# Kernel optimization log

Measured on AMD Instinct MI355X. Metric: run time of the kernel, lower is better.

## Reference

```python
import jax, jax.numpy as jnp
import numpy as np

N = 50000      # nodes
E = 800000     # edges (before self-loops)
H = 4          # attention heads
C = 32         # out_features per head
DIN = 128      # in_features (== H*C so residual path is active)
ED = 16        # edge_dim
NEG = 0.2      # LeakyReLU negative slope (GATConv default)
EPS = 1e-5     # LayerNorm eps


def setup_inputs() -> dict:
    key = jax.random.key(0)
    ks = jax.random.split(key, 12)
    s = 0.05
    return {
        "x": jax.random.normal(ks[0], (N, DIN), dtype=jnp.float32),
        "edge_index": jax.random.randint(ks[1], (2, E), 0, N, dtype=jnp.int64),
        "edge_attr": jax.random.normal(ks[2], (E, ED), dtype=jnp.float32),
        # edge_processor: Linear(ED, ED) + ReLU (dropout = identity at eval)
        "W_ep": jax.random.normal(ks[3], (ED, ED), dtype=jnp.float32) * s,
        "b_ep": jnp.zeros((ED,), dtype=jnp.float32),
        # GATConv params (lin / lin_edge are bias-free in PyG)
        "W_lin": jax.random.normal(ks[4], (DIN, H * C), dtype=jnp.float32) * s,
        "W_edge": jax.random.normal(ks[5], (ED, H * C), dtype=jnp.float32) * s,
        "att_src": jax.random.normal(ks[6], (H, C), dtype=jnp.float32) * s,
        "att_dst": jax.random.normal(ks[7], (H, C), dtype=jnp.float32) * s,
        "att_edge": jax.random.normal(ks[8], (H, C), dtype=jnp.float32) * s,
        "bias": jnp.zeros((H * C,), dtype=jnp.float32),
        # LayerNorm params
        "ln_g": jnp.ones((H * C,), dtype=jnp.float32),
        "ln_b": jnp.zeros((H * C,), dtype=jnp.float32),
    }


def reference(x, edge_index, edge_attr, W_ep, b_ep, W_lin, W_edge,
              att_src, att_dst, att_edge, bias, ln_g, ln_b):
    n = x.shape[0]
    src, dst = edge_index[0], edge_index[1]

    # edge_processor: Linear + ReLU
    ea = jax.nn.relu(edge_attr @ W_ep + b_ep)                       # [E, ED]

    # add self-loops (PyG GATConv default), loop edge_attr = mean of incoming
    ones = jnp.ones((ea.shape[0],), dtype=ea.dtype)
    deg = jax.ops.segment_sum(ones, dst, num_segments=n)            # [N]
    loop_attr = jax.ops.segment_sum(ea, dst, num_segments=n)
    loop_attr = loop_attr / jnp.maximum(deg, 1.0)[:, None]          # [N, ED]
    loop = jnp.arange(n, dtype=src.dtype)
    src2 = jnp.concatenate([src, loop])                             # [E+N]
    dst2 = jnp.concatenate([dst, loop])
    ea2 = jnp.concatenate([ea, loop_attr], axis=0)                  # [E+N, ED]

    # node / edge linear transforms
    h = (x @ W_lin).reshape(n, H, C)                                # [N, H, C]
    a_src = jnp.einsum('nhc,hc->nh', h, att_src)                    # [N, H]
    a_dst = jnp.einsum('nhc,hc->nh', h, att_dst)
    e = (ea2 @ W_edge).reshape(-1, H, C)                            # [E+N, H, C]
    a_e = jnp.einsum('ehc,hc->eh', e, att_edge)                     # [E+N, H]

    # per-edge attention logits + leaky relu
    alpha = a_src[src2] + a_dst[dst2] + a_e                         # [E+N, H]
    alpha = jnp.where(alpha >= 0, alpha, NEG * alpha)

    # segment softmax over incoming edges of each dst node
    m = jax.ops.segment_max(alpha, dst2, num_segments=n)            # [N, H]
    ex = jnp.exp(alpha - m[dst2])
    denom = jax.ops.segment_sum(ex, dst2, num_segments=n)           # [N, H]
    w = ex / denom[dst2]                                            # [E+N, H]

    # scatter-aggregate messages
    msg = h[src2] * w[:, :, None]                                   # [E+N, H, C]
    out = jax.ops.segment_sum(msg, dst2, num_segments=n)            # [N, H, C]
    out = out.reshape(n, H * C) + bias

    # residual (DIN == H*C) + LayerNorm
    out = out + x
    mu = jnp.mean(out, axis=-1, keepdims=True)
    var = jnp.var(out, axis=-1, keepdims=True)
    out = (out - mu) * jax.lax.rsqrt(var + EPS) * ln_g + ln_b
    return out
```

## Files before the change

### kernel.cpp

```cpp
#include <hip/hip_runtime.h>
#include <hip/hip_fp16.h>
#include <math.h>

#define NN   50000
#define EE   800000
#define HH   4
#define CC   32
#define DINN 128
#define ED   16
#define NEGS 0.2f
#define LNEPS 1e-5f
#define CPAD 32
#define SLOT 64
#define SLOTP (SLOT + 4)

struct __align__(16) Hp4 { __half2 a, b, c, d; };

__global__ __launch_bounds__(256, 4) void k_node(
        const float* __restrict__ x, const float* __restrict__ W_lin,
        const float* __restrict__ att_src, const float* __restrict__ att_dst,
        __half* __restrict__ hb, float* __restrict__ a_src, float* __restrict__ a_dst,
        int* __restrict__ cnt) {
    __shared__ float xr[64 * 132];
    int t = threadIdx.x;
    int row0 = blockIdx.x * 64;

    #pragma unroll
    for (int i = 0; i < 8; ++i) {
        int idx = blockIdx.x * 2048 + i * 256 + t;
        if (idx < NN * CPAD) cnt[idx] = 0;
    }

    #pragma unroll
    for (int i = 0; i < 8; ++i) {
        int idx = t + 256 * i;
        int r = idx >> 5, kq = idx & 31;
        int row = row0 + r;
        float4 v = make_float4(0.f, 0.f, 0.f, 0.f);
        if (row < NN) v = ((const float4*)x)[(long)row * 32 + kq];
        *(float4*)&xr[r * 132 + kq * 4] = v;
    }
    __syncthreads();

    int colg = t & 15, rowg = t >> 4;
    int c0 = colg * 8;
    const float* Wp = W_lin + c0;
    float acc[4][8] = {};

    #pragma unroll 2
    for (int k = 0; k < DINN; k += 2) {
        float4 wa0 = *(const float4*)&Wp[(long)k * DINN];
        float4 wb0 = *(const float4*)&Wp[(long)k * DINN + 4];
        float4 wa1 = *(const float4*)&Wp[(long)(k + 1) * DINN];
        float4 wb1 = *(const float4*)&Wp[(long)(k + 1) * DINN + 4];
        #pragma unroll
        for (int i = 0; i < 4; ++i) {
            float2 xv = *(const float2*)&xr[(rowg * 4 + i) * 132 + k];
            acc[i][0] = fmaf(xv.x, wa0.x, acc[i][0]);
            acc[i][1] = fmaf(xv.x, wa0.y, acc[i][1]);
            acc[i][2] = fmaf(xv.x, wa0.z, acc[i][2]);
            acc[i][3] = fmaf(xv.x, wa0.w, acc[i][3]);
            acc[i][4] = fmaf(xv.x, wb0.x, acc[i][4]);
            acc[i][5] = fmaf(xv.x, wb0.y, acc[i][5]);
            acc[i][6] = fmaf(xv.x, wb0.z, acc[i][6]);
            acc[i][7] = fmaf(xv.x, wb0.w, acc[i][7]);
            acc[i][0] = fmaf(xv.y, wa1.x, acc[i][0]);
            acc[i][1] = fmaf(xv.y, wa1.y, acc[i][1]);
            acc[i][2] = fmaf(xv.y, wa1.z, acc[i][2]);
            acc[i][3] = fmaf(xv.y, wa1.w, acc[i][3]);
            acc[i][4] = fmaf(xv.y, wb1.x, acc[i][4]);
            acc[i][5] = fmaf(xv.y, wb1.y, acc[i][5]);
            acc[i][6] = fmaf(xv.y, wb1.z, acc[i][6]);
            acc[i][7] = fmaf(xv.y, wb1.w, acc[i][7]);
        }
    }

    int head = colg >> 2;
    int cw = c0 & 31;
    float4 as0 = *(const float4*)&att_src[head * CC + cw];
    float4 as1 = *(const float4*)&att_src[head * CC + cw + 4];
    float4 ad0 = *(const float4*)&att_dst[head * CC + cw];
    float4 ad1 = *(const float4*)&att_dst[head * CC + cw + 4];
    #pragma unroll
    for (int i = 0; i < 4; ++i) {
        int row = row0 + rowg * 4 + i;
        if (row < NN) {
            Hp4 p;
            p.a = __floats2half2_rn(acc[i][0], acc[i][1]);
            p.b = __floats2half2_rn(acc[i][2], acc[i][3]);
            p.c = __floats2half2_rn(acc[i][4], acc[i][5]);
            p.d = __floats2half2_rn(acc[i][6], acc[i][7]);
            *(Hp4*)&hb[(long)row * DINN + c0] = p;
        }
        float ps = acc[i][0]*as0.x + acc[i][1]*as0.y + acc[i][2]*as0.z + acc[i][3]*as0.w
                 + acc[i][4]*as1.x + acc[i][5]*as1.y + acc[i][6]*as1.z + acc[i][7]*as1.w;
        float pd = acc[i][0]*ad0.x + acc[i][1]*ad0.y + acc[i][2]*ad0.z + acc[i][3]*ad0.w
                 + acc[i][4]*ad1.x + acc[i][5]*ad1.y + acc[i][6]*ad1.z + acc[i][7]*ad1.w;
        ps += __shfl_xor(ps, 1); ps += __shfl_xor(ps, 2);
        pd += __shfl_xor(pd, 1); pd += __shfl_xor(pd, 2);
        if ((colg & 3) == 0 && row < NN) {
            a_src[row * 4 + head] = ps;
            a_dst[row * 4 + head] = pd;
        }
    }
}

__device__ __forceinline__ void edge_compute(
        float4 A0, float4 A1, float4 A2, float4 A3,
        const float* __restrict__ Wl, const float* __restrict__ bl,
        const float* __restrict__ vl,
        int e, uint2* __restrict__ payload) {
    float a[ED];
    a[0]=A0.x; a[1]=A0.y; a[2]=A0.z; a[3]=A0.w;
    a[4]=A1.x; a[5]=A1.y; a[6]=A1.z; a[7]=A1.w;
    a[8]=A2.x; a[9]=A2.y; a[10]=A2.z; a[11]=A2.w;
    a[12]=A3.x; a[13]=A3.y; a[14]=A3.z; a[15]=A3.w;

    float r[ED];
    #pragma unroll
    for (int j = 0; j < ED; ++j) r[j] = bl[j];
    #pragma unroll
    for (int d = 0; d < ED; ++d) {
        float av = a[d];
        #pragma unroll
        for (int j = 0; j < ED; ++j) r[j] = fmaf(av, Wl[d * ED + j], r[j]);
    }

    float ae0 = 0.f, ae1 = 0.f, ae2 = 0.f, ae3 = 0.f;
    #pragma unroll
    for (int d = 0; d < ED; ++d) {
        float rd = fmaxf(r[d], 0.f);
        ae0 = fmaf(rd, vl[d * 4 + 0], ae0);
        ae1 = fmaf(rd, vl[d * 4 + 1], ae1);
        ae2 = fmaf(rd, vl[d * 4 + 2], ae2);
        ae3 = fmaf(rd, vl[d * 4 + 3], ae3);
    }

    __half2 ae01 = __floats2half2_rn(ae0, ae1);
    __half2 ae23 = __floats2half2_rn(ae2, ae3);
    payload[e] = make_uint2(*(unsigned*)&ae01, *(unsigned*)&ae23);
}

__global__ __launch_bounds__(256) void k_edgeA(
        const int* __restrict__ ei, const float* __restrict__ edge_attr,
        const float* __restrict__ W_ep, const float* __restrict__ b_ep,
        const float* __restrict__ W_edge, const float* __restrict__ att_edge,
        int* __restrict__ cnt, uint2* __restrict__ payload,
        uint2* __restrict__ bkt) {
    __shared__ float Wl[ED * ED];
    __shared__ float bl[ED];
    __shared__ float vl[ED * 4];
    int t = threadIdx.x;
    if (t < ED * ED) Wl[t] = W_ep[t];
    if (t < ED) bl[t] = b_ep[t];
    if (t >= 192 && t < 192 + 64) {
        int q = t - 192;
        int d = q >> 2, h = q & 3;
        float s = 0.f;
        #pragma unroll 8
        for (int c = 0; c < CC; ++c)
            s += W_edge[d * (HH * CC) + h * CC + c] * att_edge[h * CC + c];
        vl[q] = s;
    }
    __syncthreads();

    int e0 = blockIdx.x * 512 + t;
    int e1 = e0 + 256;

    if ((blockIdx.x + 1) * 512 <= EE) {
        int s0 = ei[e0], s1 = ei[e1];
        int d0 = ei[EE + e0], d1 = ei[EE + e1];

        const float4* ap0 = (const float4*)(edge_attr + (long)e0 * ED);
        const float4* ap1 = (const float4*)(edge_attr + (long)e1 * ED);
        float4 A0 = ap0[0], A1 = ap0[1], A2 = ap0[2], A3 = ap0[3];
        float4 B0 = ap1[0], B1 = ap1[1], B2 = ap1[2], B3 = ap1[3];

        int rk0 = atomicAdd(cnt + (long)d0 * CPAD, 1);
        int rk1 = atomicAdd(cnt + (long)d1 * CPAD, 1);

        if (rk0 < SLOT) bkt[(long)d0 * SLOT + rk0] = make_uint2((unsigned)e0, (unsigned)s0);
        if (rk1 < SLOT) bkt[(long)d1 * SLOT + rk1] = make_uint2((unsigned)e1, (unsigned)s1);

        edge_compute(A0, A1, A2, A3, Wl, bl, vl, e0, payload);
        edge_compute(B0, B1, B2, B3, Wl, bl, vl, e1, payload);
    } else {
        #pragma unroll
        for (int u = 0; u < 2; ++u) {
            int e = e0 + u * 256;
            if (e >= EE) break;
            int src = ei[e];
            int dst = ei[EE + e];
            const float4* ap = (const float4*)(edge_attr + (long)e * ED);
            float4 A0 = ap[0], A1 = ap[1], A2 = ap[2], A3 = ap[3];
            int rk = atomicAdd(cnt + (long)dst * CPAD, 1);
            if (rk < SLOT) bkt[(long)dst * SLOT + rk] = make_uint2((unsigned)e, (unsigned)src);
            edge_compute(A0, A1, A2, A3, Wl, bl, vl, e, payload);
        }
    }
}

__global__ __launch_bounds__(256) void k_aggregate(
        const float* __restrict__ x, const __half2* __restrict__ hb,
        const float* __restrict__ a_src, const float* __restrict__ a_dst,
        const int* __restrict__ cnt, const uint2* __restrict__ payload,
        const uint2* __restrict__ bkt,
        const float* __restrict__ bias, const float* __restrict__ ln_g,
        const float* __restrict__ ln_b, float* __restrict__ out) {
    __shared__ float2 wa[4][HH][SLOTP];
    __shared__ int    sl[4][SLOT];
    int t = threadIdx.x;
    int wave = t >> 6, lane = t & 63;
    int n = blockIdx.x * 4 + wave;

    int deg = cnt[(long)n * CPAD];
    if (deg > SLOT) deg = SLOT;
    int head = lane >> 4;

    float4 ad4 = *(const float4*)&a_dst[n * 4];

    if (lane < deg) {
        uint2 b = bkt[(long)n * SLOT + lane];
        int eidx = (int)b.x;
        int src  = (int)b.y;
        uint2 q = payload[eidx];
        float4 as4 = *(const float4*)&a_src[src * 4];
        float2 a01 = __half22float2(*(__half2*)&q.x);
        float2 a23 = __half22float2(*(__half2*)&q.y);
        float v0 = as4.x + ad4.x + a01.x; v0 = (v0 >= 0.f) ? v0 : NEGS * v0;
        float v1 = as4.y + ad4.y + a01.y; v1 = (v1 >= 0.f) ? v1 : NEGS * v1;
        float v2 = as4.z + ad4.z + a23.x; v2 = (v2 >= 0.f) ? v2 : NEGS * v2;
        float v3 = as4.w + ad4.w + a23.y; v3 = (v3 >= 0.f) ? v3 : NEGS * v3;
        wa[wave][0][lane] = make_float2(__expf(v0), a01.x);
        wa[wave][1][lane] = make_float2(__expf(v1), a01.y);
        wa[wave][2][lane] = make_float2(__expf(v2), a23.x);
        wa[wave][3][lane] = make_float2(__expf(v3), a23.y);
        sl[wave][lane] = src;
    }
    __syncthreads();

    const float2* wp = &wa[wave][head][0];
    const int*    sp = &sl[wave][0];
    float accx = 0.f, accy = 0.f, s_own = 0.f, aes_own = 0.f;

    int k = 0;
    for (; k + 8 <= deg; k += 8) {
        int s0 = sp[k+0], s1 = sp[k+1], s2 = sp[k+2], s3 = sp[k+3];
        int s4 = sp[k+4], s5 = sp[k+5], s6 = sp[k+6], s7 = sp[k+7];
        float2 W0 = wp[k+0], W1 = wp[k+1], W2 = wp[k+2], W3 = wp[k+3];
        float2 W4 = wp[k+4], W5 = wp[k+5], W6 = wp[k+6], W7 = wp[k+7];
        __half2 h0 = hb[(long)s0 * 64 + lane], h1 = hb[(long)s1 * 64 + lane];
        __half2 h2 = hb[(long)s2 * 64 + lane], h3 = hb[(long)s3 * 64 + lane];
        __half2 h4 = hb[(long)s4 * 64 + lane], h5 = hb[(long)s5 * 64 + lane];
        __half2 h6 = hb[(long)s6 * 64 + lane], h7 = hb[(long)s7 * 64 + lane];
        float2 f0 = __half22float2(h0), f1 = __half22float2(h1);
        float2 f2 = __half22float2(h2), f3 = __half22float2(h3);
        float2 f4 = __half22float2(h4), f5 = __half22float2(h5);
        float2 f6 = __half22float2(h6), f7 = __half22float2(h7);
        s_own += W0.x; aes_own += W0.y;
        accx = fmaf(W0.x, f0.x, accx); accy = fmaf(W0.x, f0.y, accy);
        s_own += W1.x; aes_own += W1.y;
        accx = fmaf(W1.x, f1.x, accx); accy = fmaf(W1.x, f1.y, accy);
        s_own += W2.x; aes_own += W2.y;
        accx = fmaf(W2.x, f2.x, accx); accy = fmaf(W2.x, f2.y, accy);
        s_own += W3.x; aes_own += W3.y;
        accx = fmaf(W3.x, f3.x, accx); accy = fmaf(W3.x, f3.y, accy);
        s_own += W4.x; aes_own += W4.y;
        accx = fmaf(W4.x, f4.x, accx); accy = fmaf(W4.x, f4.y, accy);
        s_own += W5.x; aes_own += W5.y;
        accx = fmaf(W5.x, f5.x, accx); accy = fmaf(W5.x, f5.y, accy);
        s_own += W6.x; aes_own += W6.y;
        accx = fmaf(W6.x, f6.x, accx); accy = fmaf(W6.x, f6.y, accy);
        s_own += W7.x; aes_own += W7.y;
        accx = fmaf(W7.x, f7.x, accx); accy = fmaf(W7.x, f7.y, accy);
    }
    for (; k < deg; ++k) {
        int s0 = sp[k];
        float2 W0 = wp[k];
        __half2 h0 = hb[(long)s0 * 64 + lane];
        float2 f0 = __half22float2(h0);
        s_own += W0.x; aes_own += W0.y;
        accx = fmaf(W0.x, f0.x, accx); accy = fmaf(W0.x, f0.y, accy);
    }

    float adn = (head & 2) ? ((head & 1) ? ad4.w : ad4.z)
                           : ((head & 1) ? ad4.y : ad4.x);
    float asn = a_src[n * 4 + head];
    float inv_deg = 1.0f / fmaxf((float)deg, 1.0f);
    float v = asn + adn + aes_own * inv_deg;
    v = (v >= 0.f) ? v : NEGS * v;
    float w0 = __expf(v);
    s_own += w0;
    float2 hn = __half22float2(hb[(long)n * 64 + lane]);
    accx = fmaf(w0, hn.x, accx);
    accy = fmaf(w0, hn.y, accy);
    float is = 1.0f / s_own;
    accx *= is; accy *= is;

    int c0 = lane * 2;
    float2 b2 = *(const float2*)&bias[c0];
    float2 x2 = *(const float2*)&x[(long)n * DINN + c0];
    float oa = accx + b2.x + x2.x;
    float ob = accy + b2.y + x2.y;
    float sum = oa + ob, sumsq = oa * oa + ob * ob;
    #pragma unroll
    for (int d2 = 1; d2 < 64; d2 <<= 1) {
        sum   += __shfl_xor(sum, d2);
        sumsq += __shfl_xor(sumsq, d2);
    }
    float mu  = sum * (1.0f / DINN);
    float var = sumsq * (1.0f / DINN) - mu * mu;
    float rs  = rsqrtf(var + LNEPS);
    float2 g2  = *(const float2*)&ln_g[c0];
    float2 lb2 = *(const float2*)&ln_b[c0];
    float2 o2;
    o2.x = (oa - mu) * rs * g2.x + lb2.x;
    o2.y = (ob - mu) * rs * g2.y + lb2.y;
    *(float2*)&out[(long)n * DINN + c0] = o2;
}

extern "C" void kernel_launch(void* const* d_in, const int* in_sizes, int n_in,
                              void* d_out, int out_size, void* d_ws, size_t ws_size,
                              hipStream_t stream) {
    const float* x         = (const float*)d_in[0];
    const int*   ei        = (const int*)d_in[1];
    const float* edge_attr = (const float*)d_in[2];
    const float* W_ep      = (const float*)d_in[3];
    const float* b_ep      = (const float*)d_in[4];
    const float* W_lin     = (const float*)d_in[5];
    const float* W_edge    = (const float*)d_in[6];
    const float* att_src   = (const float*)d_in[7];
    const float* att_dst   = (const float*)d_in[8];
    const float* att_edge  = (const float*)d_in[9];
    const float* bias      = (const float*)d_in[10];
    const float* ln_g      = (const float*)d_in[11];
    const float* ln_b      = (const float*)d_in[12];
    float* out = (float*)d_out;

    char* ws = (char*)d_ws;
    size_t o = 0;
    auto take = [&](size_t bytes) -> char* {
        char* p = ws + o;
        o = (o + bytes + 255) & ~(size_t)255;
        return p;
    };
    __half* hbuf    = (__half*)take((size_t)NN * DINN * 2);
    float*  a_src   = (float*)take((size_t)NN * 4 * 4);
    float*  a_dst   = (float*)take((size_t)NN * 4 * 4);
    int*    cnt     = (int*)  take((size_t)NN * CPAD * 4);
    uint2*  payload = (uint2*)take((size_t)EE * 8);
    uint2*  bkt     = (uint2*)take((size_t)NN * SLOT * 8);

    k_node<<<(NN + 63) / 64, 256, 0, stream>>>(x, W_lin, att_src, att_dst,
                                               hbuf, a_src, a_dst, cnt);
    k_edgeA<<<(EE + 511) / 512, 256, 0, stream>>>(ei, edge_attr, W_ep, b_ep,
                                                  W_edge, att_edge, cnt,
                                                  payload, bkt);
    k_aggregate<<<(NN + 3) / 4, 256, 0, stream>>>(x, (const __half2*)hbuf,
                                                  a_src, a_dst, cnt,
                                                  payload, bkt,
                                                  bias, ln_g, ln_b, out);
}
```

Baseline: 255.6 us.

## Fuse edge MLP attention logit computation into aggregation kernel

The per-edge Linear+ReLU and attention-edge projection moves out of the bucketing kernel and into the aggregation kernel. Each gathered incoming edge now reads its raw edge_attr row and computes its logit in place, so the fp16 payload array no longer has to be written and then read back. The bucketing kernel shrinks to index loads and atomics only. In exchange, aggregation does a random 64-byte gather per edge instead of an 8-byte one, and its register pressure rises from the 16x16 MLP.

```diff
diff --git a/kernel.cpp b/kernel.cpp
--- a/kernel.cpp
+++ b/kernel.cpp
@@ -105,52 +105,51 @@
     }
 }
 
-__device__ __forceinline__ void edge_compute(
-        float4 A0, float4 A1, float4 A2, float4 A3,
-        const float* __restrict__ Wl, const float* __restrict__ bl,
-        const float* __restrict__ vl,
-        int e, uint2* __restrict__ payload) {
-    float a[ED];
-    a[0]=A0.x; a[1]=A0.y; a[2]=A0.z; a[3]=A0.w;
-    a[4]=A1.x; a[5]=A1.y; a[6]=A1.z; a[7]=A1.w;
-    a[8]=A2.x; a[9]=A2.y; a[10]=A2.z; a[11]=A2.w;
-    a[12]=A3.x; a[13]=A3.y; a[14]=A3.z; a[15]=A3.w;
-
-    float r[ED];
-    #pragma unroll
-    for (int j = 0; j < ED; ++j) r[j] = bl[j];
-    #pragma unroll
-    for (int d = 0; d < ED; ++d) {
-        float av = a[d];
-        #pragma unroll
-        for (int j = 0; j < ED; ++j) r[j] = fmaf(av, Wl[d * ED + j], r[j]);
-    }
-
-    float ae0 = 0.f, ae1 = 0.f, ae2 = 0.f, ae3 = 0.f;
-    #pragma unroll
-    for (int d = 0; d < ED; ++d) {
-        float rd = fmaxf(r[d], 0.f);
-        ae0 = fmaf(rd, vl[d * 4 + 0], ae0);
-        ae1 = fmaf(rd, vl[d * 4 + 1], ae1);
-        ae2 = fmaf(rd, vl[d * 4 + 2], ae2);
-        ae3 = fmaf(rd, vl[d * 4 + 3], ae3);
-    }
-
-    __half2 ae01 = __floats2half2_rn(ae0, ae1);
-    __half2 ae23 = __floats2half2_rn(ae2, ae3);
-    payload[e] = make_uint2(*(unsigned*)&ae01, *(unsigned*)&ae23);
+__global__ __launch_bounds__(256) void k_bkt(
+        const int* __restrict__ ei, int* __restrict__ cnt,
+        uint2* __restrict__ bkt) {
+    int t = threadIdx.x;
+    int e0 = blockIdx.x * 512 + t;
+    int e1 = e0 + 256;
+
+    if ((blockIdx.x + 1) * 512 <= EE) {
+        int s0 = ei[e0], s1 = ei[e1];
+        int d0 = ei[EE + e0], d1 = ei[EE + e1];
+        int rk0 = atomicAdd(cnt + (long)d0 * CPAD, 1);
+        int rk1 = atomicAdd(cnt + (long)d1 * CPAD, 1);
+        if (rk0 < SLOT) bkt[(long)d0 * SLOT + rk0] = make_uint2((unsigned)e0, (unsigned)s0);
+        if (rk1 < SLOT) bkt[(long)d1 * SLOT + rk1] = make_uint2((unsigned)e1, (unsigned)s1);
+    } else {
+        #pragma unroll
+        for (int u = 0; u < 2; ++u) {
+            int e = e0 + u * 256;
+            if (e >= EE) break;
+            int src = ei[e];
+            int dst = ei[EE + e];
+            int rk = atomicAdd(cnt + (long)dst * CPAD, 1);
+            if (rk < SLOT) bkt[(long)dst * SLOT + rk] = make_uint2((unsigned)e, (unsigned)src);
+        }
+    }
 }
 
-__global__ __launch_bounds__(256) void k_edgeA(
-        const int* __restrict__ ei, const float* __restrict__ edge_attr,
+__global__ __launch_bounds__(256) void k_aggregate(
+        const float* __restrict__ x, const __half2* __restrict__ hb,
+        const float* __restrict__ a_src, const float* __restrict__ a_dst,
+        const int* __restrict__ cnt, const float* __restrict__ edge_attr,
+        const uint2* __restrict__ bkt,
         const float* __restrict__ W_ep, const float* __restrict__ b_ep,
         const float* __restrict__ W_edge, const float* __restrict__ att_edge,
-        int* __restrict__ cnt, uint2* __restrict__ payload,
-        uint2* __restrict__ bkt) {
-    __shared__ float Wl[ED * ED];
-    __shared__ float bl[ED];
-    __shared__ float vl[ED * 4];
+        const float* __restrict__ bias, const float* __restrict__ ln_g,
+        const float* __restrict__ ln_b, float* __restrict__ out) {
+    __shared__ float2 wa[4][HH][SLOTP];
+    __shared__ int    sl[4][SLOT];
+    __shared__ float  Wl[ED * ED];
+    __shared__ float  bl[ED];
+    __shared__ float  vl[ED * 4];
     int t = threadIdx.x;
+    int wave = t >> 6, lane = t & 63;
+    int n = blockIdx.x * 4 + wave;
+
     if (t < ED * ED) Wl[t] = W_ep[t];
     if (t < ED) bl[t] = b_ep[t];
     if (t >= 192 && t < 192 + 64) {
@@ -162,79 +161,56 @@
             s += W_edge[d * (HH * CC) + h * CC + c] * att_edge[h * CC + c];
         vl[q] = s;
     }
-    __syncthreads();
-
-    int e0 = blockIdx.x * 512 + t;
-    int e1 = e0 + 256;
-
-    if ((blockIdx.x + 1) * 512 <= EE) {
-        int s0 = ei[e0], s1 = ei[e1];
-        int d0 = ei[EE + e0], d1 = ei[EE + e1];
-
-        const float4* ap0 = (const float4*)(edge_attr + (long)e0 * ED);
-        const float4* ap1 = (const float4*)(edge_attr + (long)e1 * ED);
-        float4 A0 = ap0[0], A1 = ap0[1], A2 = ap0[2], A3 = ap0[3];
-        float4 B0 = ap1[0], B1 = ap1[1], B2 = ap1[2], B3 = ap1[3];
-
-        int rk0 = atomicAdd(cnt + (long)d0 * CPAD, 1);
-        int rk1 = atomicAdd(cnt + (long)d1 * CPAD, 1);
-
-        if (rk0 < SLOT) bkt[(long)d0 * SLOT + rk0] = make_uint2((unsigned)e0, (unsigned)s0);
-        if (rk1 < SLOT) bkt[(long)d1 * SLOT + rk1] = make_uint2((unsigned)e1, (unsigned)s1);
-
-        edge_compute(A0, A1, A2, A3, Wl, bl, vl, e0, payload);
-        edge_compute(B0, B1, B2, B3, Wl, bl, vl, e1, payload);
-    } else {
-        #pragma unroll
-        for (int u = 0; u < 2; ++u) {
-            int e = e0 + u * 256;
-            if (e >= EE) break;
-            int src = ei[e];
-            int dst = ei[EE + e];
-            const float4* ap = (const float4*)(edge_attr + (long)e * ED);
-            float4 A0 = ap[0], A1 = ap[1], A2 = ap[2], A3 = ap[3];
-            int rk = atomicAdd(cnt + (long)dst * CPAD, 1);
-            if (rk < SLOT) bkt[(long)dst * SLOT + rk] = make_uint2((unsigned)e, (unsigned)src);
-            edge_compute(A0, A1, A2, A3, Wl, bl, vl, e, payload);
-        }
-    }
-}
-
-__global__ __launch_bounds__(256) void k_aggregate(
-        const float* __restrict__ x, const __half2* __restrict__ hb,
-        const float* __restrict__ a_src, const float* __restrict__ a_dst,
-        const int* __restrict__ cnt, const uint2* __restrict__ payload,
-        const uint2* __restrict__ bkt,
-        const float* __restrict__ bias, const float* __restrict__ ln_g,
-        const float* __restrict__ ln_b, float* __restrict__ out) {
-    __shared__ float2 wa[4][HH][SLOTP];
-    __shared__ int    sl[4][SLOT];
-    int t = threadIdx.x;
-    int wave = t >> 6, lane = t & 63;
-    int n = blockIdx.x * 4 + wave;
 
     int deg = cnt[(long)n * CPAD];
     if (deg > SLOT) deg = SLOT;
     int head = lane >> 4;
 
     float4 ad4 = *(const float4*)&a_dst[n * 4];
+    __syncthreads();
 
     if (lane < deg) {
         uint2 b = bkt[(long)n * SLOT + lane];
         int eidx = (int)b.x;
         int src  = (int)b.y;
-        uint2 q = payload[eidx];
+        const float4* ap = (const float4*)(edge_attr + (long)eidx * ED);
+        float4 A0 = ap[0], A1 = ap[1], A2 = ap[2], A3 = ap[3];
         float4 as4 = *(const float4*)&a_src[src * 4];
-        float2 a01 = __half22float2(*(__half2*)&q.x);
-        float2 a23 = __half22float2(*(__half2*)&q.y);
-        float v0 = as4.x + ad4.x + a01.x; v0 = (v0 >= 0.f) ? v0 : NEGS * v0;
-        float v1 = as4.y + ad4.y + a01.y; v1 = (v1 >= 0.f) ? v1 : NEGS * v1;
-        float v2 = as4.z + ad4.z + a23.x; v2 = (v2 >= 0.f) ? v2 : NEGS * v2;
-        float v3 = as4.w + ad4.w + a23.y; v3 = (v3 >= 0.f) ? v3 : NEGS * v3;
-        wa[wave][0][lane] = make_float2(__expf(v0), a01.x);
-        wa[wave][1][lane] = make_float2(__expf(v1), a01.y);
-        wa[wave][2][lane] = make_float2(__expf(v2), a23.x);
-        wa[wave][3][lane] = make_float2(__expf(v3), a23.y);
+
+        float a[ED];
+        a[0]=A0.x; a[1]=A0.y; a[2]=A0.z; a[3]=A0.w;
+        a[4]=A1.x; a[5]=A1.y; a[6]=A1.z; a[7]=A1.w;
+        a[8]=A2.x; a[9]=A2.y; a[10]=A2.z; a[11]=A2.w;
+        a[12]=A3.x; a[13]=A3.y; a[14]=A3.z; a[15]=A3.w;
+
+        float r[ED];
+        #pragma unroll
+        for (int j = 0; j < ED; ++j) r[j] = bl[j];
+        #pragma unroll
+        for (int d = 0; d < ED; ++d) {
+            float av = a[d];
+            #pragma unroll
+            for (int j = 0; j < ED; ++j) r[j] = fmaf(av, Wl[d * ED + j], r[j]);
+        }
+
+        float ae0 = 0.f, ae1 = 0.f, ae2 = 0.f, ae3 = 0.f;
+        #pragma unroll
+        for (int d = 0; d < ED; ++d) {
+            float rd = fmaxf(r[d], 0.f);
+            ae0 = fmaf(rd, vl[d * 4 + 0], ae0);
+            ae1 = fmaf(rd, vl[d * 4 + 1], ae1);
+            ae2 = fmaf(rd, vl[d * 4 + 2], ae2);
+            ae3 = fmaf(rd, vl[d * 4 + 3], ae3);
+        }
+
+        float v0 = as4.x + ad4.x + ae0; v0 = (v0 >= 0.f) ? v0 : NEGS * v0;
+        float v1 = as4.y + ad4.y + ae1; v1 = (v1 >= 0.f) ? v1 : NEGS * v1;
+        float v2 = as4.z + ad4.z + ae2; v2 = (v2 >= 0.f) ? v2 : NEGS * v2;
+        float v3 = as4.w + ad4.w + ae3; v3 = (v3 >= 0.f) ? v3 : NEGS * v3;
+        wa[wave][0][lane] = make_float2(__expf(v0), ae0);
+        wa[wave][1][lane] = make_float2(__expf(v1), ae1);
+        wa[wave][2][lane] = make_float2(__expf(v2), ae2);
+        wa[wave][3][lane] = make_float2(__expf(v3), ae3);
         sl[wave][lane] = src;
     }
     __syncthreads();
@@ -344,20 +320,18 @@
         o = (o + bytes + 255) & ~(size_t)255;
         return p;
     };
-    __half* hbuf    = (__half*)take((size_t)NN * DINN * 2);
-    float*  a_src   = (float*)take((size_t)NN * 4 * 4);
-    float*  a_dst   = (float*)take((size_t)NN * 4 * 4);
-    int*    cnt     = (int*)  take((size_t)NN * CPAD * 4);
-    uint2*  payload = (uint2*)take((size_t)EE * 8);
-    uint2*  bkt     = (uint2*)take((size_t)NN * SLOT * 8);
+    __half* hbuf  = (__half*)take((size_t)NN * DINN * 2);
+    float*  a_src = (float*)take((size_t)NN * 4 * 4);
+    float*  a_dst = (float*)take((size_t)NN * 4 * 4);
+    int*    cnt   = (int*)  take((size_t)NN * CPAD * 4);
+    uint2*  bkt   = (uint2*)take((size_t)NN * SLOT * 8);
 
     k_node<<<(NN + 63) / 64, 256, 0, stream>>>(x, W_lin, att_src, att_dst,
                                                hbuf, a_src, a_dst, cnt);
-    k_edgeA<<<(EE + 511) / 512, 256, 0, stream>>>(ei, edge_attr, W_ep, b_ep,
-                                                  W_edge, att_edge, cnt,
-                                                  payload, bkt);
+    k_bkt<<<(EE + 511) / 512, 256, 0, stream>>>(ei, cnt, bkt);
     k_aggregate<<<(NN + 3) / 4, 256, 0, stream>>>(x, (const __half2*)hbuf,
                                                   a_src, a_dst, cnt,
-                                                  payload, bkt,
+                                                  edge_attr, bkt,
+                                                  W_ep, b_ep, W_edge, att_edge,
                                                   bias, ln_g, ln_b, out);
 }
```

Result: slower. 282.8 us (+10.6%).
